# Optimization experiments

Measured on AMD Instinct MI355X. Metric: run time of the kernel, lower is better.

## Reference

```python
import jax, jax.numpy as jnp
import numpy as np

B, THETA_DIM, Y_DIM, OUT_DIM, WIDTH, NUM_BLOCKS, MULT = 16384, 64, 16, 256, 1024, 4, 2
EPS = 1e-5


def setup_inputs() -> dict:
    key = jax.random.key(0)
    ks = jax.random.split(key, 16)
    hid = MULT * WIDTH
    in_dim = THETA_DIM + 1 + Y_DIM
    inp = {
        "theta_n": jax.random.normal(ks[0], (B, THETA_DIM), jnp.float32),
        "lambda_n": jax.random.normal(ks[1], (B, 1), jnp.float32),
        "y_oh": jax.random.uniform(ks[2], (B, Y_DIM), jnp.float32),
        # input layer
        "W_in": jax.random.normal(ks[3], (in_dim, WIDTH), jnp.float32) * 0.02,
        "b_in": jnp.zeros((WIDTH,), jnp.float32),
        # stacked ResBlockLN params [num_blocks, ...]
        "ln_g": jnp.ones((NUM_BLOCKS, WIDTH), jnp.float32),
        "ln_b": jnp.zeros((NUM_BLOCKS, WIDTH), jnp.float32),
        "w1": jax.random.normal(ks[4], (NUM_BLOCKS, WIDTH, hid), jnp.float32) * 0.02,
        "b1": jnp.zeros((NUM_BLOCKS, hid), jnp.float32),
        "w2": jax.random.normal(ks[5], (NUM_BLOCKS, hid, WIDTH), jnp.float32) * 0.02,
        "b2": jnp.zeros((NUM_BLOCKS, WIDTH), jnp.float32),
        "res_scale": jnp.full((NUM_BLOCKS,), 0.1, jnp.float32),
        # per-class heads stacked [y_dim, width, out_dim]
        "Wh": jax.random.normal(ks[6], (Y_DIM, WIDTH, OUT_DIM), jnp.float32) * 0.02,
        "bh": jnp.zeros((Y_DIM, OUT_DIM), jnp.float32),
    }
    return inp


def _layernorm(x, g, b):
    mu = jnp.mean(x, axis=-1, keepdims=True)
    var = jnp.mean(jnp.square(x - mu), axis=-1, keepdims=True)
    return (x - mu) * jax.lax.rsqrt(var + EPS) * g + b


def reference(theta_n, lambda_n, y_oh, W_in, b_in, ln_g, ln_b, w1, b1, w2, b2, res_scale, Wh, bh):
    x = jnp.concatenate([theta_n, lambda_n, y_oh], axis=1)  # [B, theta+1+y]
    h = jax.nn.gelu(x @ W_in + b_in, approximate=False)      # [B, width]
    for i in range(NUM_BLOCKS):
        z = _layernorm(h, ln_g[i], ln_b[i])
        z = jax.nn.silu(z @ w1[i] + b1[i])
        z = z @ w2[i] + b2[i]
        h = h + res_scale[i] * z
    y_int = jnp.argmax(y_oh, axis=1)                         # [B]
    # compute all heads, then per-sample gather (argmax-routed head)
    all_out = jnp.einsum("bd,kdo->bko", h, Wh) + bh          # [B, y_dim, out_dim]
    out = jnp.take_along_axis(all_out, y_int[:, None, None], axis=1)[:, 0, :]
    return out
```

## Files before the change

### kernel.cpp

```cpp
#include <hip/hip_runtime.h>
#include <hip/hip_bf16.h>
#include <cstdint>
#include <cstddef>

#define B_ROWS 16384
#define WIDTH  1024
#define HID    2048
#define NBLK   4
#define YDIM   16
#define OUTD   256
#define KIN    128
#define MAXM_PER_CLASS 4096

typedef __attribute__((ext_vector_type(8))) short short8;
typedef __attribute__((ext_vector_type(4))) float f32x4;

__device__ __forceinline__ unsigned short f2bf(float f) {
    union { float f; uint32_t u; } v; v.f = f;
    uint32_t u = v.u;
    uint32_t r = (u + 0x7FFFu + ((u >> 16) & 1u)) >> 16;
    return (unsigned short)r;
}

__device__ __forceinline__ void gload_lds16(const void* g, void* l) {
    __builtin_amdgcn_global_load_lds(
        (const __attribute__((address_space(1))) void*)g,
        (__attribute__((address_space(3))) void*)l, 16, 0, 0);
}

__global__ __launch_bounds__(256)
void prep_x_k(const float* __restrict__ theta, const float* __restrict__ lam,
              const float* __restrict__ yoh, unsigned short* __restrict__ xb)
{
    int tid = threadIdx.x;
    int row = blockIdx.x * 2 + (tid >> 7);
    int j = tid & 127;
    float v;
    if (j < 64)       v = theta[(size_t)row * 64 + j];
    else if (j == 64) v = lam[row];
    else if (j < 81)  v = yoh[(size_t)row * 16 + (j - 65)];
    else              v = 0.f;
    xb[(size_t)row * KIN + j] = f2bf(v);
}

__global__ __launch_bounds__(256)
void bucket_k(const float* __restrict__ yoh, int* __restrict__ counts,
              int* __restrict__ bucket)
{
    __shared__ int cnt_lds[16];
    __shared__ int base_lds[16];
    int tid = threadIdx.x;
    if (tid < 16) cnt_lds[tid] = 0;
    __syncthreads();
    int row = blockIdx.x * 256 + tid;
    const float4* yr = (const float4*)(yoh + (size_t)row * 16);
    int best = 0; float bv = -3.0e38f;
    #pragma unroll
    for (int p = 0; p < 4; ++p) {
        float4 v = yr[p];
        if (v.x > bv) { bv = v.x; best = p * 4 + 0; }
        if (v.y > bv) { bv = v.y; best = p * 4 + 1; }
        if (v.z > bv) { bv = v.z; best = p * 4 + 2; }
        if (v.w > bv) { bv = v.w; best = p * 4 + 3; }
    }
    int mypos = atomicAdd(&cnt_lds[best], 1);
    __syncthreads();
    if (tid < 16) base_lds[tid] = atomicAdd(&counts[tid * 32], cnt_lds[tid]);
    __syncthreads();
    int pos = base_lds[best] + mypos;
    if (pos < MAXM_PER_CLASS) bucket[best * MAXM_PER_CLASS + pos] = row;
}

__global__ __launch_bounds__(256)
void tcvt_k(const float* __restrict__ src, unsigned short* __restrict__ dst,
            int R, int C, int RP)
{
    int b = blockIdx.z;
    src += (size_t)b * R * C;
    dst += (size_t)b * C * RP;
    __shared__ float tile[32][33];
    int tx = threadIdx.x & 31, ty = threadIdx.x >> 5;
    int c0 = blockIdx.x * 32, r0 = blockIdx.y * 32;
    #pragma unroll
    for (int p = 0; p < 4; ++p) {
        int r = r0 + p * 8 + ty;
        float v = (r < R) ? src[(size_t)r * C + c0 + tx] : 0.f;
        tile[p * 8 + ty][tx] = v;
    }
    __syncthreads();
    #pragma unroll
    for (int p = 0; p < 4; ++p) {
        int c = c0 + p * 8 + ty;
        dst[(size_t)c * RP + r0 + tx] = f2bf(tile[tx][p * 8 + ty]);
    }
}

__global__ __launch_bounds__(256)
void ln_k(const float* __restrict__ h, const float* __restrict__ g,
          const float* __restrict__ bb, unsigned short* __restrict__ z)
{
    int row = blockIdx.x;
    int t = threadIdx.x;
    const float4 v = ((const float4*)(h + (size_t)row * WIDTH))[t];
    float s  = v.x + v.y + v.z + v.w;
    float s2 = v.x * v.x + v.y * v.y + v.z * v.z + v.w * v.w;
    #pragma unroll
    for (int off = 32; off > 0; off >>= 1) {
        s  += __shfl_down(s, off);
        s2 += __shfl_down(s2, off);
    }
    __shared__ float red[8];
    int wv = t >> 6;
    if ((t & 63) == 0) { red[wv] = s; red[4 + wv] = s2; }
    __syncthreads();
    float st = 0.f, s2t = 0.f;
    #pragma unroll
    for (int i = 0; i < 4; ++i) { st += red[i]; s2t += red[4 + i]; }
    float mu  = st * (1.f / 1024.f);
    float var = s2t * (1.f / 1024.f) - mu * mu;
    float rs  = rsqrtf(var + 1e-5f);
    float4 gg  = ((const float4*)g)[t];
    float4 bbv = ((const float4*)bb)[t];
    ushort4 o;
    o.x = f2bf((v.x - mu) * rs * gg.x + bbv.x);
    o.y = f2bf((v.y - mu) * rs * gg.y + bbv.y);
    o.z = f2bf((v.z - mu) * rs * gg.z + bbv.z);
    o.w = f2bf((v.w - mu) * rs * gg.w + bbv.w);
    ((ushort4*)(z + (size_t)row * WIDTH))[t] = o;
}

template<int EPI>
__global__ __launch_bounds__(256)
void gemm_k(const short* __restrict__ A, const short* __restrict__ BT,
            const float* __restrict__ bias,
            float* __restrict__ Cf, unsigned short* __restrict__ Cb,
            const float* __restrict__ rs_ptr, int rs_idx, int writeHb,
            const int* __restrict__ counts, const int* __restrict__ bucket,
            float* __restrict__ outp,
            int N, int K, int ntN)
{
    __shared__ short lsA[128 * 64];
    __shared__ short lsB[128 * 64];
    __shared__ int rowsLds[128];

    int tid = threadIdx.x;
    int w = tid >> 6, lane = tid & 63;

    int bm = 0, bn = 0, m0 = 0, cnt = 0;
    if (EPI == 3) {
        int cls = blockIdx.z;
        cnt = counts[cls * 32];
        if (cnt > MAXM_PER_CLASS) cnt = MAXM_PER_CLASS;
        m0 = blockIdx.y * 128;
        if (m0 >= cnt) return;
        bn = blockIdx.x;
        if (tid < 128) rowsLds[tid] = bucket[cls * MAXM_PER_CLASS + m0 + tid];
        __syncthreads();
        BT   += (size_t)cls * OUTD * WIDTH;
        bias += cls * OUTD;
    } else {
        int nwg = gridDim.x;
        int wg  = blockIdx.x;
        int cpx = nwg >> 3;
        int swz = (wg & 7) * cpx + (wg >> 3);
        bm = swz / ntN; bn = swz % ntN;
    }

    const int sr = lane >> 3;
    const int ss = lane & 7;

    f32x4 acc[4][4];
    #pragma unroll
    for (int i = 0; i < 4; ++i)
        #pragma unroll
        for (int j = 0; j < 4; ++j) acc[i][j] = (f32x4)(0.f);

    const int wm = w >> 1, wn = w & 1;
    const int nkt = K >> 6;

    for (int kt = 0; kt < nkt; ++kt) {
        #pragma unroll
        for (int c = 0; c < 4; ++c) {
            int r  = w * 32 + c * 8 + sr;
            int sg = ss ^ (r & 7);
            long grow = (EPI == 3) ? (long)rowsLds[r] : ((long)bm * 128 + r);
            const short* ga = A + (size_t)grow * K + kt * 64 + sg * 8;
            gload_lds16(ga, &lsA[(w * 32 + c * 8) * 64]);
        }
        #pragma unroll
        for (int c = 0; c < 4; ++c) {
            int r  = w * 32 + c * 8 + sr;
            int sg = ss ^ (r & 7);
            const short* gb = BT + (size_t)(bn * 128 + r) * K + kt * 64 + sg * 8;
            gload_lds16(gb, &lsB[(w * 32 + c * 8) * 64]);
        }
        __syncthreads();
        #pragma unroll
        for (int ks = 0; ks < 2; ++ks) {
            short8 af[4], bf[4];
            #pragma unroll
            for (int m = 0; m < 4; ++m) {
                int r = wm * 64 + m * 16 + (lane & 15);
                int s = ks * 4 + (lane >> 4);
                af[m] = *(const short8*)&lsA[r * 64 + (s ^ (r & 7)) * 8];
            }
            #pragma unroll
            for (int n = 0; n < 4; ++n) {
                int r = wn * 64 + n * 16 + (lane & 15);
                int s = ks * 4 + (lane >> 4);
                bf[n] = *(const short8*)&lsB[r * 64 + (s ^ (r & 7)) * 8];
            }
            #pragma unroll
            for (int m = 0; m < 4; ++m)
                #pragma unroll
                for (int n = 0; n < 4; ++n)
                    acc[m][n] = __builtin_amdgcn_mfma_f32_16x16x32_bf16(af[m], bf[n], acc[m][n], 0, 0, 0);
        }
        __syncthreads();
    }

    float rscale = (EPI == 2) ? rs_ptr[rs_idx] : 0.f;
    #pragma unroll
    for (int m = 0; m < 4; ++m) {
        #pragma unroll
        for (int reg = 0; reg < 4; ++reg) {
            int lr = wm * 64 + m * 16 + (lane >> 4) * 4 + reg;
            #pragma unroll
            for (int n = 0; n < 4; ++n) {
                int lc = wn * 64 + n * 16 + (lane & 15);
                float v = acc[m][n][reg];
                if (EPI == 0) {
                    size_t idx = ((size_t)bm * 128 + lr) * (size_t)N + bn * 128 + lc;
                    float x = v + bias[bn * 128 + lc];
                    Cf[idx] = 0.5f * x * (1.f + erff(x * 0.70710678118f));
                } else if (EPI == 1) {
                    size_t idx = ((size_t)bm * 128 + lr) * (size_t)N + bn * 128 + lc;
                    float x = v + bias[bn * 128 + lc];
                    Cb[idx] = f2bf(x / (1.f + __expf(-x)));
                } else if (EPI == 2) {
                    size_t idx = ((size_t)bm * 128 + lr) * (size_t)N + bn * 128 + lc;
                    float x = v + bias[bn * 128 + lc];
                    float hv = Cf[idx] + rscale * x;
                    Cf[idx] = hv;
                    if (writeHb) Cb[idx] = f2bf(hv);
                } else {
                    if (m0 + lr < cnt) {
                        int orow = rowsLds[lr];
                        int oc = bn * 128 + lc;
                        outp[(size_t)orow * OUTD + oc] = v + bias[oc];
                    }
                }
            }
        }
    }
}

extern "C" void kernel_launch(void* const* d_in, const int* in_sizes, int n_in,
                              void* d_out, int out_size, void* d_ws, size_t ws_size,
                              hipStream_t stream)
{
    const float* theta = (const float*)d_in[0];
    const float* lam   = (const float*)d_in[1];
    const float* yoh   = (const float*)d_in[2];
    const float* W_in  = (const float*)d_in[3];
    const float* b_in  = (const float*)d_in[4];
    const float* ln_g  = (const float*)d_in[5];
    const float* ln_b  = (const float*)d_in[6];
    const float* w1    = (const float*)d_in[7];
    const float* b1    = (const float*)d_in[8];
    const float* w2    = (const float*)d_in[9];
    const float* b2    = (const float*)d_in[10];
    const float* rsc   = (const float*)d_in[11];
    const float* Wh    = (const float*)d_in[12];
    const float* bh    = (const float*)d_in[13];
    float* out = (float*)d_out;

    char* p = (char*)d_ws;
    auto alloc = [&](size_t bytes) -> char* {
        char* r = p; p += (bytes + 255) & ~(size_t)255; return r;
    };
    float*          h    = (float*)         alloc((size_t)B_ROWS * WIDTH * 4);
    unsigned short* hb   = (unsigned short*)alloc((size_t)B_ROWS * WIDTH * 2);
    unsigned short* z    = (unsigned short*)alloc((size_t)B_ROWS * WIDTH * 2);
    unsigned short* t    = (unsigned short*)alloc((size_t)B_ROWS * HID * 2);
    unsigned short* xb   = (unsigned short*)alloc((size_t)B_ROWS * KIN * 2);
    unsigned short* w1T  = (unsigned short*)alloc((size_t)NBLK * HID * WIDTH * 2);
    unsigned short* w2T  = (unsigned short*)alloc((size_t)NBLK * WIDTH * HID * 2);
    unsigned short* WhT  = (unsigned short*)alloc((size_t)YDIM * OUTD * WIDTH * 2);
    unsigned short* WiT  = (unsigned short*)alloc((size_t)WIDTH * KIN * 2);
    int*            bucket = (int*)alloc((size_t)YDIM * MAXM_PER_CLASS * 4);
    int*            counts = (int*)alloc(16 * 32 * 4);

    hipMemsetAsync(bucket, 0, (size_t)YDIM * MAXM_PER_CLASS * 4, stream);
    hipMemsetAsync(counts, 0, 16 * 32 * 4, stream);

    prep_x_k<<<B_ROWS / 2, 256, 0, stream>>>(theta, lam, yoh, xb);
    bucket_k<<<B_ROWS / 256, 256, 0, stream>>>(yoh, counts, bucket);

    tcvt_k<<<dim3(WIDTH / 32, KIN / 32, 1),    256, 0, stream>>>(W_in, WiT, 81,   WIDTH, KIN);
    tcvt_k<<<dim3(HID / 32,   WIDTH / 32, 4),  256, 0, stream>>>(w1,   w1T, WIDTH, HID,  WIDTH);
    tcvt_k<<<dim3(WIDTH / 32, HID / 32, 4),    256, 0, stream>>>(w2,   w2T, HID,  WIDTH, HID);
    tcvt_k<<<dim3(OUTD / 32,  WIDTH / 32, 16), 256, 0, stream>>>(Wh,   WhT, WIDTH, OUTD, WIDTH);

    gemm_k<0><<<(B_ROWS / 128) * (WIDTH / 128), 256, 0, stream>>>(
        (const short*)xb, (const short*)WiT, b_in, h, nullptr,
        nullptr, 0, 0, nullptr, nullptr, nullptr, WIDTH, KIN, WIDTH / 128);

    for (int i = 0; i < NBLK; ++i) {
        ln_k<<<B_ROWS, 256, 0, stream>>>(h, ln_g + i * WIDTH, ln_b + i * WIDTH, z);
        gemm_k<1><<<(B_ROWS / 128) * (HID / 128), 256, 0, stream>>>(
            (const short*)z, (const short*)(w1T + (size_t)i * HID * WIDTH), b1 + i * HID,
            nullptr, t, nullptr, 0, 0, nullptr, nullptr, nullptr, HID, WIDTH, HID / 128);
        gemm_k<2><<<(B_ROWS / 128) * (WIDTH / 128), 256, 0, stream>>>(
            (const short*)t, (const short*)(w2T + (size_t)i * WIDTH * HID), b2 + i * WIDTH,
            h, hb, rsc, i, (i == NBLK - 1) ? 1 : 0, nullptr, nullptr, nullptr,
            WIDTH, HID, WIDTH / 128);
    }

    gemm_k<3><<<dim3(OUTD / 128, MAXM_PER_CLASS / 128, YDIM), 256, 0, stream>>>(
        (const short*)hb, (const short*)WhT, bh, nullptr, nullptr,
        nullptr, 0, 0, counts, bucket, out, OUTD, WIDTH, OUTD / 128);

    (void)in_sizes; (void)n_in; (void)out_size; (void)ws_size; (void)rsc;
}
```

Measured before the change: 1.119 ms.

## Double-buffer LDS tiles in GEMM to overlap global loads with MFMA

```diff
diff --git a/kernel.cpp b/kernel.cpp
--- a/kernel.cpp
+++ b/kernel.cpp
@@ -139,8 +139,8 @@
             float* __restrict__ outp,
             int N, int K, int ntN)
 {
-    __shared__ short lsA[128 * 64];
-    __shared__ short lsB[128 * 64];
+    __shared__ short lsA[2][128 * 64];
+    __shared__ short lsB[2][128 * 64];
     __shared__ int rowsLds[128];
 
     int tid = threadIdx.x;
@@ -168,33 +168,41 @@
 
     const int sr = lane >> 3;
     const int ss = lane & 7;
-
-    f32x4 acc[4][4];
-    #pragma unroll
-    for (int i = 0; i < 4; ++i)
-        #pragma unroll
-        for (int j = 0; j < 4; ++j) acc[i][j] = (f32x4)(0.f);
-
     const int wm = w >> 1, wn = w & 1;
     const int nkt = K >> 6;
 
-    for (int kt = 0; kt < nkt; ++kt) {
+    f32x4 acc[4][4];
+    #pragma unroll
+    for (int i = 0; i < 4; ++i)
+        #pragma unroll
+        for (int j = 0; j < 4; ++j) acc[i][j] = (f32x4)(0.f);
+
+    auto STAGE = [&](int buf, int kt) {
         #pragma unroll
         for (int c = 0; c < 4; ++c) {
             int r  = w * 32 + c * 8 + sr;
             int sg = ss ^ (r & 7);
             long grow = (EPI == 3) ? (long)rowsLds[r] : ((long)bm * 128 + r);
-            const short* ga = A + (size_t)grow * K + kt * 64 + sg * 8;
-            gload_lds16(ga, &lsA[(w * 32 + c * 8) * 64]);
+            const short* ga = A + (size_t)grow * K + (size_t)kt * 64 + sg * 8;
+            gload_lds16(ga, &lsA[buf][(w * 32 + c * 8) * 64]);
         }
         #pragma unroll
         for (int c = 0; c < 4; ++c) {
             int r  = w * 32 + c * 8 + sr;
             int sg = ss ^ (r & 7);
-            const short* gb = BT + (size_t)(bn * 128 + r) * K + kt * 64 + sg * 8;
-            gload_lds16(gb, &lsB[(w * 32 + c * 8) * 64]);
+            const short* gb = BT + (size_t)(bn * 128 + r) * K + (size_t)kt * 64 + sg * 8;
+            gload_lds16(gb, &lsB[buf][(w * 32 + c * 8) * 64]);
         }
-        __syncthreads();
+    };
+
+    STAGE(0, 0);
+    asm volatile("s_waitcnt vmcnt(0)" ::: "memory");
+    __builtin_amdgcn_s_barrier();
+
+    int cur = 0;
+    for (int kt = 0; kt < nkt; ++kt) {
+        if (kt + 1 < nkt) STAGE(cur ^ 1, kt + 1);
+
         #pragma unroll
         for (int ks = 0; ks < 2; ++ks) {
             short8 af[4], bf[4];
@@ -202,21 +210,26 @@
             for (int m = 0; m < 4; ++m) {
                 int r = wm * 64 + m * 16 + (lane & 15);
                 int s = ks * 4 + (lane >> 4);
-                af[m] = *(const short8*)&lsA[r * 64 + (s ^ (r & 7)) * 8];
+                af[m] = *(const short8*)&lsA[cur][r * 64 + (s ^ (r & 7)) * 8];
             }
             #pragma unroll
             for (int n = 0; n < 4; ++n) {
                 int r = wn * 64 + n * 16 + (lane & 15);
                 int s = ks * 4 + (lane >> 4);
-                bf[n] = *(const short8*)&lsB[r * 64 + (s ^ (r & 7)) * 8];
+                bf[n] = *(const short8*)&lsB[cur][r * 64 + (s ^ (r & 7)) * 8];
             }
+            __builtin_amdgcn_s_setprio(1);
             #pragma unroll
             for (int m = 0; m < 4; ++m)
                 #pragma unroll
                 for (int n = 0; n < 4; ++n)
                     acc[m][n] = __builtin_amdgcn_mfma_f32_16x16x32_bf16(af[m], bf[n], acc[m][n], 0, 0, 0);
+            __builtin_amdgcn_s_setprio(0);
         }
-        __syncthreads();
+
+        asm volatile("s_waitcnt vmcnt(0)" ::: "memory");
+        __builtin_amdgcn_s_barrier();
+        cur ^= 1;
     }
 
     float rscale = (EPI == 2) ? rs_ptr[rs_idx] : 0.f;
```

Result: faster. 1.058 ms (-5.5%).
